# Kernel optimization log

Hardware: AMD Instinct MI355X
Metric: run time of the kernel (lower is better)

The kernel has to match this reference:

```python
import jax, jax.numpy as jnp
import numpy as np
from jax import lax

H = 2048          # hidden_size
T = 365           # history_length
F = 90            # future_u_length
TARGET_STEP = 30
RECOVER = 0.05
DEATH = 0.01


def setup_inputs() -> dict:
    key = jax.random.key(0)
    ks = jax.random.split(key, 14)
    s = 1.0 / np.sqrt(H)
    u = lambda k, shape: jax.random.uniform(k, shape, minval=-s, maxval=s, dtype=jnp.float32)
    return {
        "history_u": jax.random.uniform(ks[0], (1, 1, T), dtype=jnp.float32),
        "sird": jax.random.uniform(ks[1], (1, 1, 5), minval=0.5, maxval=1.5, dtype=jnp.float32),
        "target_step": TARGET_STEP,
        "Wb": u(ks[2], (H, 1)), "bb": u(ks[3], (H,)),
        "enc_Wih": u(ks[4], (3 * H, H)), "enc_Whh": u(ks[5], (3 * H, H)),
        "enc_bih": u(ks[6], (3 * H,)), "enc_bhh": u(ks[7], (3 * H,)),
        "dec_Wih": u(ks[8], (3 * H, H)), "dec_Whh": u(ks[9], (3 * H, H)),
        "dec_bih": u(ks[10], (3 * H,)), "dec_bhh": u(ks[11], (3 * H,)),
        "Wa": u(ks[12], (1, H)), "ba": u(ks[13], (1,)),
    }


def _gru_cell(x, h, Wih, Whh, bih, bhh):
    # PyTorch GRU cell math; x, h are [H] vectors.
    n = h.shape[0]
    gi = Wih @ x + bih            # [3H]
    gh = Whh @ h + bhh            # [3H]
    r = jax.nn.sigmoid(gi[:n] + gh[:n])
    z = jax.nn.sigmoid(gi[n:2 * n] + gh[n:2 * n])
    c = jnp.tanh(gi[2 * n:] + r * gh[2 * n:])
    return (1.0 - z) * c + z * h


def reference(history_u, sird, target_step, Wb, bb,
              enc_Wih, enc_Whh, enc_bih, enc_bhh,
              dec_Wih, dec_Whh, dec_bih, dec_bhh, Wa, ba):
    hsz = bb.shape[0]
    # Pre-projection of scalar inputs: [T, H]
    xs = history_u[0, 0][:, None] @ Wb.T + bb

    def enc_step(h, x):
        hp = _gru_cell(x, h, enc_Wih, enc_Whh, enc_bih, enc_bhh)
        # original applies sigmoid to hidden state between steps, keeps raw hp as y
        return jax.nn.sigmoid(hp), hp

    h_enc, ys = lax.scan(enc_step, jnp.zeros((hsz,), dtype=xs.dtype), xs)
    y = ys[-1]

    def dec_step(carry, _):
        y, h = carry
        hp = _gru_cell(y, h, dec_Wih, dec_Whh, dec_bih, dec_bhh)
        beta = jax.nn.sigmoid(hp @ Wa[0] + ba[0])   # scalar
        return (hp, hp), beta

    _, betas = lax.scan(dec_step, (y, h_enc), None, length=F)   # [F]

    def sird_update(x, beta):
        s, i, r, d, n = x[0], x[1], x[2], x[3], x[4]
        si = s * i * beta / n
        ir = i * RECOVER
        idd = i * DEATH
        return jnp.stack([s - si, i + si - ir - idd, r + ir, d + idd, n])

    x0 = sird[0, 0]
    xF = lax.scan(lambda x, b: (sird_update(x, b), None), x0, betas)[0]

    beta_last = betas[-1]

    def const_step(x, _):
        x2 = sird_update(x, beta_last)
        return x2, x2

    x_final, x_foo = lax.scan(const_step, xF, None, length=target_step - 1)
    return x_final.reshape(1, 1, 5), x_foo.reshape(-1, 1, 1, 5)
```

## Files before the change

kernel.cpp:

```cpp
#include <hip/hip_runtime.h>
#include <hip/hip_fp16.h>
#include <cstdint>
#include <cstddef>


#define HID   2048
#define T_ENC 365
#define F_DEC 90
#define NWG   256
#define NTH   512
#define SLOT  8192

#define WS_P    0
#define WS_Q    6144
#define WS_HBUF 12288
#define WS_DX0  45056
#define WS_HST  61440

typedef unsigned long long u64;

__device__ __forceinline__ float sigm(float x) {
    return 1.0f / (1.0f + __expf(-x));
}
__device__ __forceinline__ float tanh_f(float x) {
    return 1.0f - 2.0f / (1.0f + __expf(2.0f * x));
}
__device__ __forceinline__ unsigned bf16rne(float f) {
    unsigned x = __float_as_uint(f);
    return (x + 0x7fffu + ((x >> 16) & 1u)) >> 16;
}
__device__ __forceinline__ unsigned packbf(float lo, float hi) {
    return bf16rne(lo) | (bf16rne(hi) << 16);
}

__device__ __forceinline__ u64 tld(const u64* p) {
    return __hip_atomic_load((u64*)p, __ATOMIC_RELAXED, __HIP_MEMORY_SCOPE_AGENT);
}
__device__ __forceinline__ void tst(u64* p, u64 v) {
    __hip_atomic_store(p, v, __ATOMIC_RELAXED, __HIP_MEMORY_SCOPE_AGENT);
}
__device__ __forceinline__ u64 mk16(unsigned tag, float lo, float hi) {
    unsigned pk = (unsigned)__half_as_ushort(__float2half(lo)) |
                  ((unsigned)__half_as_ushort(__float2half(hi)) << 16);
    return ((u64)tag << 32) | (u64)pk;
}

__device__ __forceinline__ void poll_to_lds(const u64* __restrict__ rep,
                                            unsigned tag, int tid,
                                            float* __restrict__ lds) {
    const u64* p0 = rep + tid;
    const u64* p1 = rep + 512 + tid;
    u64 x0, x1;
    while (true) {
        x0 = tld(p0);
        x1 = tld(p1);
        bool ok = ((unsigned)(x0 >> 32) == tag) & ((unsigned)(x1 >> 32) == tag);
        if (__ballot(ok) == ~0ull) break;
    }
    unsigned lo0 = (unsigned)x0, lo1 = (unsigned)x1;
    float2 f0 = __half22float2(*(__half2*)&lo0);
    float2 f1 = __half22float2(*(__half2*)&lo1);
    *(float2*)(lds + 2 * tid) = f0;
    *(float2*)(lds + 1024 + 2 * tid) = f1;
}

__global__ void prep_pq(const float* __restrict__ Wih, const float* __restrict__ Wb,
                        const float* __restrict__ bb, const float* __restrict__ bih,
                        float* __restrict__ p, float* __restrict__ q) {
    int wave = threadIdx.x >> 6, lane = threadIdx.x & 63;
    int row = blockIdx.x * 4 + wave;
    const float* wr = Wih + (size_t)row * HID;
    float ap = 0.f, aq = 0.f;
    for (int k = lane; k < HID; k += 64) {
        float w = wr[k];
        ap += w * Wb[k];
        aq += w * bb[k];
    }
#pragma unroll
    for (int m = 1; m < 64; m <<= 1) {
        ap += __shfl_xor(ap, m);
        aq += __shfl_xor(aq, m);
    }
    if (lane == 0) {
        p[row] = ap;
        q[row] = aq + bih[row];
    }
}

__global__ __launch_bounds__(NTH, 1) void persist(
    const float* __restrict__ hu, const float* __restrict__ encWhh,
    const float* __restrict__ encBhh, const float* __restrict__ decWih,
    const float* __restrict__ decWhh, const float* __restrict__ decBih,
    const float* __restrict__ decBhh, const float* __restrict__ p,
    const float* __restrict__ q, u64* hbuf, u64* dx0, __half* hstore) {
    const int wg = blockIdx.x, tid = threadIdx.x;
    const int wave = tid >> 6, lane = tid & 63;
    const int j = wg * 8 + wave;
    const int myrep = wg & 7;

    __shared__ float h_lds[HID], x_lds[HID];
    __shared__ float hs_l[8], hy_l[8];
    __shared__ float p_l[24], q_l[24], ebhh[24], dbih[24], dbhh[24];
    __shared__ float u_l[T_ENC];

    for (int idx = tid; idx < T_ENC; idx += NTH) u_l[idx] = hu[idx];
    if (tid < 24) {
        int g = tid >> 3, jj = tid & 7;
        int r = g * HID + wg * 8 + jj;
        p_l[tid] = p[r];
        q_l[tid] = q[r];
        ebhh[tid] = encBhh[r];
        dbih[tid] = decBih[r];
        dbhh[tid] = decBhh[r];
    }

    float4 We[3][8];
#pragma unroll
    for (int g = 0; g < 3; g++) {
        const float* base = encWhh + (size_t)(g * HID + j) * HID;
#pragma unroll
        for (int i = 0; i < 8; i++)
            We[g][i] = *reinterpret_cast<const float4*>(base + 4 * lane + 256 * i);
    }

    for (int t = 0; t < T_ENC; t++) {
        if (t == 0) {
            for (int idx = tid; idx < HID; idx += NTH) h_lds[idx] = 0.f;
        } else {
            poll_to_lds(hbuf + (t & 1) * SLOT + myrep * 1024, (unsigned)t, tid,
                        h_lds);
        }
        __syncthreads();

        float4 hreg[8];
#pragma unroll
        for (int i = 0; i < 8; i++)
            hreg[i] = *reinterpret_cast<const float4*>(&h_lds[4 * lane + 256 * i]);

        float v0, v1, v2;
        {
            float a0 = 0.f, a1 = 0.f, a2 = 0.f, a3 = 0.f;
            float b0 = 0.f, b1 = 0.f, b2 = 0.f, b3 = 0.f;
            float c0 = 0.f, c1 = 0.f, c2 = 0.f, c3 = 0.f;
#pragma unroll
            for (int i = 0; i < 8; i++) {
                float4 h4 = hreg[i];
                float4 wr_ = We[0][i], wz_ = We[1][i], wc_ = We[2][i];
                a0 += wr_.x * h4.x; a1 += wr_.y * h4.y;
                a2 += wr_.z * h4.z; a3 += wr_.w * h4.w;
                b0 += wz_.x * h4.x; b1 += wz_.y * h4.y;
                b2 += wz_.z * h4.z; b3 += wz_.w * h4.w;
                c0 += wc_.x * h4.x; c1 += wc_.y * h4.y;
                c2 += wc_.z * h4.z; c3 += wc_.w * h4.w;
            }
            v0 = (a0 + a1) + (a2 + a3);
            v1 = (b0 + b1) + (b2 + b3);
            v2 = (c0 + c1) + (c2 + c3);
        }
#pragma unroll
        for (int m = 1; m < 64; m <<= 1) {
            v0 += __shfl_xor(v0, m);
            v1 += __shfl_xor(v1, m);
            v2 += __shfl_xor(v2, m);
        }

        if (lane == 0) {
            float u = u_l[t];
            float gir = u * p_l[wave] + q_l[wave];
            float giz = u * p_l[8 + wave] + q_l[8 + wave];
            float gic = u * p_l[16 + wave] + q_l[16 + wave];
            float r = sigm(gir + v0 + ebhh[wave]);
            float z = sigm(giz + v1 + ebhh[8 + wave]);
            float c = tanh_f(gic + r * (v2 + ebhh[16 + wave]));
            float hp = (1.f - z) * c + z * h_lds[j];
            hs_l[wave] = sigm(hp);
            hy_l[wave] = hp;
        }
        __syncthreads();
        if (wave == 0 && lane < 32) {
            int i = lane & 3, r = lane >> 2;
            u64 v = mk16((unsigned)(t + 1), hs_l[2 * i], hs_l[2 * i + 1]);
            tst(hbuf + ((t + 1) & 1) * SLOT + r * 1024 + wg * 4 + i, v);
            if (t == T_ENC - 1) {
                u64 y = mk16((unsigned)T_ENC, hy_l[2 * i], hy_l[2 * i + 1]);
                tst(dx0 + r * 1024 + wg * 4 + i, y);
            }
        }
    }

    unsigned Wd[6][8][2];
#pragma unroll
    for (int g = 0; g < 6; g++) {
        const float* src = (g < 3)
            ? decWih + (size_t)(g * HID + j) * HID
            : decWhh + (size_t)((g - 3) * HID + j) * HID;
#pragma unroll
        for (int i = 0; i < 8; i++) {
            float4 w = *reinterpret_cast<const float4*>(src + 4 * lane + 256 * i);
            Wd[g][i][0] = packbf(w.x, w.y);
            Wd[g][i][1] = packbf(w.z, w.w);
        }
    }

    for (int s = 0; s < F_DEC; s++) {
        unsigned rt = (unsigned)(T_ENC + s);
        poll_to_lds(hbuf + (rt & 1) * SLOT + myrep * 1024, rt, tid, h_lds);
        if (s == 0) poll_to_lds(dx0 + myrep * 1024, (unsigned)T_ENC, tid, x_lds);
        __syncthreads();

        const float* xs = (s == 0) ? x_lds : h_lds;
        float4 vx[8], vh[8];
#pragma unroll
        for (int i = 0; i < 8; i++) {
            vx[i] = *reinterpret_cast<const float4*>(&xs[4 * lane + 256 * i]);
            vh[i] = *reinterpret_cast<const float4*>(&h_lds[4 * lane + 256 * i]);
        }

        float d[6];
#pragma unroll
        for (int g = 0; g < 6; g++) {
            float a0 = 0.f, a1 = 0.f, a2 = 0.f, a3 = 0.f;
#pragma unroll
            for (int i = 0; i < 8; i++) {
                unsigned u0 = Wd[g][i][0], u1 = Wd[g][i][1];
                float4 v4 = (g < 3) ? vx[i] : vh[i];
                a0 += __uint_as_float(u0 << 16) * v4.x;
                a1 += __uint_as_float(u0 & 0xffff0000u) * v4.y;
                a2 += __uint_as_float(u1 << 16) * v4.z;
                a3 += __uint_as_float(u1 & 0xffff0000u) * v4.w;
            }
            d[g] = (a0 + a1) + (a2 + a3);
        }
#pragma unroll
        for (int m = 1; m < 64; m <<= 1) {
#pragma unroll
            for (int g = 0; g < 6; g++) d[g] += __shfl_xor(d[g], m);
        }

        if (lane == 0) {
            float r = sigm(d[0] + dbih[wave] + d[3] + dbhh[wave]);
            float z = sigm(d[1] + dbih[8 + wave] + d[4] + dbhh[8 + wave]);
            float c = tanh_f(d[2] + dbih[16 + wave] +
                             r * (d[5] + dbhh[16 + wave]));
            float hp = (1.f - z) * c + z * h_lds[j];
            hy_l[wave] = hp;
            hstore[s * HID + j] = __float2half(hp);
        }
        __syncthreads();
        if (wave == 0 && lane < 32) {
            int i = lane & 3, r = lane >> 2;
            u64 v = mk16(rt + 1, hy_l[2 * i], hy_l[2 * i + 1]);
            tst(hbuf + ((rt + 1) & 1) * SLOT + r * 1024 + wg * 4 + i, v);
        }
    }
}

__global__ void sird_k(const float* __restrict__ sird, const float* __restrict__ Wa,
                       const float* __restrict__ ba, const int* __restrict__ ts_p,
                       const __half* __restrict__ hstore, float* __restrict__ out) {
    __shared__ float bpre[96];
    int wave = threadIdx.x >> 6, lane = threadIdx.x & 63;
    const float4* wa4 = (const float4*)Wa;
    for (int s = wave; s < F_DEC; s += 8) {
        const uint4* hr = (const uint4*)(hstore + (size_t)s * HID);
        float acc = 0.f;
#pragma unroll
        for (int m = 0; m < 4; m++) {
            uint4 hh = hr[lane + 64 * m];
            float4 w0 = wa4[2 * (lane + 64 * m)];
            float4 w1 = wa4[2 * (lane + 64 * m) + 1];
            float2 f;
            f = __half22float2(*(__half2*)&hh.x);
            acc += w0.x * f.x + w0.y * f.y;
            f = __half22float2(*(__half2*)&hh.y);
            acc += w0.z * f.x + w0.w * f.y;
            f = __half22float2(*(__half2*)&hh.z);
            acc += w1.x * f.x + w1.y * f.y;
            f = __half22float2(*(__half2*)&hh.w);
            acc += w1.z * f.x + w1.w * f.y;
        }
#pragma unroll
        for (int m = 1; m < 64; m <<= 1) acc += __shfl_xor(acc, m);
        if (lane == 0) bpre[s] = acc;
    }
    __syncthreads();
    if (threadIdx.x == 0) {
        float s = sird[0], i = sird[1], r = sird[2], d = sird[3], n = sird[4];
        float bl = 0.f;
        for (int t = 0; t < F_DEC; t++) {
            float b = 1.f / (1.f + expf(-(bpre[t] + ba[0])));
            bl = b;
            float si = s * i * b / n, ir = i * 0.05f, id = i * 0.01f;
            s -= si;
            i += si - ir - id;
            r += ir;
            d += id;
        }
        int ts = ts_p[0];
        float* foo = out + 5;
        for (int t = 0; t < ts - 1; t++) {
            float si = s * i * bl / n, ir = i * 0.05f, id = i * 0.01f;
            s -= si;
            i += si - ir - id;
            r += ir;
            d += id;
            foo[t * 5 + 0] = s;
            foo[t * 5 + 1] = i;
            foo[t * 5 + 2] = r;
            foo[t * 5 + 3] = d;
            foo[t * 5 + 4] = n;
        }
        out[0] = s;
        out[1] = i;
        out[2] = r;
        out[3] = d;
        out[4] = n;
    }
}

extern "C" void kernel_launch(void* const* d_in, const int* in_sizes, int n_in,
                              void* d_out, int out_size, void* d_ws, size_t ws_size,
                              hipStream_t stream) {
    const float* hu = (const float*)d_in[0];
    const float* sird = (const float*)d_in[1];
    const int* ts = (const int*)d_in[2];
    const float* Wb = (const float*)d_in[3];
    const float* bb = (const float*)d_in[4];
    const float* eWih = (const float*)d_in[5];
    const float* eWhh = (const float*)d_in[6];
    const float* eBih = (const float*)d_in[7];
    const float* eBhh = (const float*)d_in[8];
    const float* dWih = (const float*)d_in[9];
    const float* dWhh = (const float*)d_in[10];
    const float* dBih = (const float*)d_in[11];
    const float* dBhh = (const float*)d_in[12];
    const float* Wa = (const float*)d_in[13];
    const float* ba = (const float*)d_in[14];

    float* wsf = (float*)d_ws;
    float* p = wsf + WS_P;
    float* q = wsf + WS_Q;
    u64* hbuf = (u64*)(wsf + WS_HBUF);
    u64* dx0 = (u64*)(wsf + WS_DX0);
    __half* hstore = (__half*)(wsf + WS_HST);

    hipLaunchKernelGGL(prep_pq, dim3(6144 / 4), dim3(256), 0, stream, eWih, Wb, bb,
                       eBih, p, q);
    hipLaunchKernelGGL(persist, dim3(NWG), dim3(NTH), 0, stream, hu, eWhh, eBhh,
                       dWih, dWhh, dBih, dBhh, p, q, hbuf, dx0, hstore);
    hipLaunchKernelGGL(sird_k, dim3(1), dim3(NTH), 0, stream, sird, Wa, ba, ts,
                       hstore, (float*)d_out);
}
```

Measured before the change: 1.796 ms.

## Use per-XCD leader workgroups to relay hidden state through local buffers

Each workgroup reads its XCD id from a hardware register and takes a slot from a per-XCD counter. The first workgroup on each XCD becomes a leader: it polls one global copy of the hidden state and re-publishes it into two XCD-local buffers with sc0 stores. The others poll those local copies with sc0 loads and fall back to the global buffer after a spin limit. Writers now publish a single copy instead of eight replicas. The aim is to cut cross-XCD coherence traffic during the per-step handoff, at the cost of an extra relay hop per step and a dependence on workgroups being spread evenly across XCDs.

```diff
diff --git a/kernel.cpp b/kernel.cpp
--- a/kernel.cpp
+++ b/kernel.cpp
@@ -9,13 +9,16 @@
 #define F_DEC 90
 #define NWG   256
 #define NTH   512
-#define SLOT  8192
+#define FB_SPIN 4096
 
 #define WS_P    0
 #define WS_Q    6144
-#define WS_HBUF 12288
-#define WS_DX0  45056
-#define WS_HST  61440
+#define WS_CTR  12288
+#define WS_GBUF 12296
+#define WS_GDX0 16392
+#define WS_LBUF 18440
+#define WS_LDX0 83976
+#define WS_HST  100360
 
 typedef unsigned long long u64;
 
@@ -39,17 +42,42 @@
 __device__ __forceinline__ void tst(u64* p, u64 v) {
     __hip_atomic_store(p, v, __ATOMIC_RELAXED, __HIP_MEMORY_SCOPE_AGENT);
 }
+__device__ __forceinline__ void ld2_sc0(const u64* p0, const u64* p1, u64& a,
+                                        u64& b) {
+    asm volatile(
+        "global_load_dwordx2 %0, %2, off sc0\n\t"
+        "global_load_dwordx2 %1, %3, off sc0\n\t"
+        "s_waitcnt vmcnt(0)"
+        : "=&v"(a), "=&v"(b)
+        : "v"(p0), "v"(p1)
+        : "memory");
+}
+__device__ __forceinline__ void st_sc0(u64* p, u64 v) {
+    asm volatile("global_store_dwordx2 %0, %1, off sc0" ::"v"(p), "v"(v)
+                 : "memory");
+}
+
 __device__ __forceinline__ u64 mk16(unsigned tag, float lo, float hi) {
     unsigned pk = (unsigned)__half_as_ushort(__float2half(lo)) |
                   ((unsigned)__half_as_ushort(__float2half(hi)) << 16);
     return ((u64)tag << 32) | (u64)pk;
 }
 
-__device__ __forceinline__ void poll_to_lds(const u64* __restrict__ rep,
-                                            unsigned tag, int tid,
-                                            float* __restrict__ lds) {
-    const u64* p0 = rep + tid;
-    const u64* p1 = rep + 512 + tid;
+__device__ __forceinline__ void unpack2(u64 x0, u64 x1, int tid,
+                                        float* __restrict__ lds) {
+    unsigned lo0 = (unsigned)x0, lo1 = (unsigned)x1;
+    float2 f0 = __half22float2(*(__half2*)&lo0);
+    float2 f1 = __half22float2(*(__half2*)&lo1);
+    *(float2*)(lds + 2 * tid) = f0;
+    *(float2*)(lds + 1024 + 2 * tid) = f1;
+}
+
+__device__ __forceinline__ void leader_step(const u64* __restrict__ g,
+                                            u64* __restrict__ l0,
+                                            u64* __restrict__ l1, unsigned tag,
+                                            int tid, float* __restrict__ lds) {
+    const u64* p0 = g + tid;
+    const u64* p1 = g + 512 + tid;
     u64 x0, x1;
     while (true) {
         x0 = tld(p0);
@@ -57,16 +85,53 @@
         bool ok = ((unsigned)(x0 >> 32) == tag) & ((unsigned)(x1 >> 32) == tag);
         if (__ballot(ok) == ~0ull) break;
     }
-    unsigned lo0 = (unsigned)x0, lo1 = (unsigned)x1;
-    float2 f0 = __half22float2(*(__half2*)&lo0);
-    float2 f1 = __half22float2(*(__half2*)&lo1);
-    *(float2*)(lds + 2 * tid) = f0;
-    *(float2*)(lds + 1024 + 2 * tid) = f1;
+    st_sc0(l0 + tid, x0);
+    st_sc0(l0 + 512 + tid, x1);
+    st_sc0(l1 + tid, x0);
+    st_sc0(l1 + 512 + tid, x1);
+    unpack2(x0, x1, tid, lds);
+}
+
+__device__ __forceinline__ void follower_step(const u64* __restrict__ l,
+                                              const u64* __restrict__ g,
+                                              unsigned tag, int tid,
+                                              float* __restrict__ lds,
+                                              bool& use_gb) {
+    u64 x0 = 0, x1 = 0;
+    if (!use_gb) {
+        const u64* p0 = l + tid;
+        const u64* p1 = l + 512 + tid;
+        int spins = 0;
+        while (true) {
+            ld2_sc0(p0, p1, x0, x1);
+            bool ok =
+                ((unsigned)(x0 >> 32) == tag) & ((unsigned)(x1 >> 32) == tag);
+            if (__ballot(ok) == ~0ull) break;
+            if (++spins > FB_SPIN) {
+                use_gb = true;
+                break;
+            }
+        }
+    }
+    if (use_gb) {
+        const u64* p0 = g + tid;
+        const u64* p1 = g + 512 + tid;
+        while (true) {
+            x0 = tld(p0);
+            x1 = tld(p1);
+            bool ok =
+                ((unsigned)(x0 >> 32) == tag) & ((unsigned)(x1 >> 32) == tag);
+            if (__ballot(ok) == ~0ull) break;
+        }
+    }
+    unpack2(x0, x1, tid, lds);
 }
 
 __global__ void prep_pq(const float* __restrict__ Wih, const float* __restrict__ Wb,
                         const float* __restrict__ bb, const float* __restrict__ bih,
-                        float* __restrict__ p, float* __restrict__ q) {
+                        float* __restrict__ p, float* __restrict__ q,
+                        int* __restrict__ ctr) {
+    if (blockIdx.x == 0 && threadIdx.x < 8) ctr[threadIdx.x] = 0;
     int wave = threadIdx.x >> 6, lane = threadIdx.x & 63;
     int row = blockIdx.x * 4 + wave;
     const float* wr = Wih + (size_t)row * HID;
@@ -92,16 +157,17 @@
     const float* __restrict__ encBhh, const float* __restrict__ decWih,
     const float* __restrict__ decWhh, const float* __restrict__ decBih,
     const float* __restrict__ decBhh, const float* __restrict__ p,
-    const float* __restrict__ q, u64* hbuf, u64* dx0, __half* hstore) {
+    const float* __restrict__ q, int* ctr, u64* gbuf, u64* gdx0, u64* lbuf,
+    u64* ldx0, __half* hstore) {
     const int wg = blockIdx.x, tid = threadIdx.x;
     const int wave = tid >> 6, lane = tid & 63;
     const int j = wg * 8 + wave;
-    const int myrep = wg & 7;
 
     __shared__ float h_lds[HID], x_lds[HID];
     __shared__ float hs_l[8], hy_l[8];
     __shared__ float p_l[24], q_l[24], ebhh[24], dbih[24], dbhh[24];
     __shared__ float u_l[T_ENC];
+    __shared__ int org_s[2];
 
     for (int idx = tid; idx < T_ENC; idx += NTH) u_l[idx] = hu[idx];
     if (tid < 24) {
@@ -113,6 +179,18 @@
         dbih[tid] = decBih[r];
         dbhh[tid] = decBhh[r];
     }
+    if (tid == 0) {
+        int xcd = (int)(__builtin_amdgcn_s_getreg((3 << 11) | 20)) & 7;
+        org_s[0] = xcd;
+        org_s[1] = atomicAdd(ctr + xcd, 1);
+    }
+    __syncthreads();
+    const int xcd = org_s[0];
+    const bool islead = (org_s[1] == 0);
+    const int myrep = org_s[1] & 1;
+    u64* lbx = lbuf + (size_t)xcd * 4096;
+    u64* lx0 = ldx0 + (size_t)xcd * 1024;
+    bool use_gb = false;
 
     float4 We[3][8];
 #pragma unroll
@@ -127,8 +205,14 @@
         if (t == 0) {
             for (int idx = tid; idx < HID; idx += NTH) h_lds[idx] = 0.f;
         } else {
-            poll_to_lds(hbuf + (t & 1) * SLOT + myrep * 1024, (unsigned)t, tid,
-                        h_lds);
+            const int slot = t & 1;
+            if (islead)
+                leader_step(gbuf + slot * 1024, lbx + slot * 2048,
+                            lbx + slot * 2048 + 1024, (unsigned)t, tid, h_lds);
+            else
+                follower_step(lbx + slot * 2048 + myrep * 1024,
+                              gbuf + slot * 1024, (unsigned)t, tid, h_lds,
+                              use_gb);
         }
         __syncthreads();
 
@@ -177,13 +261,12 @@
             hy_l[wave] = hp;
         }
         __syncthreads();
-        if (wave == 0 && lane < 32) {
-            int i = lane & 3, r = lane >> 2;
-            u64 v = mk16((unsigned)(t + 1), hs_l[2 * i], hs_l[2 * i + 1]);
-            tst(hbuf + ((t + 1) & 1) * SLOT + r * 1024 + wg * 4 + i, v);
+        if (wave == 0 && lane < 4) {
+            u64 v = mk16((unsigned)(t + 1), hs_l[2 * lane], hs_l[2 * lane + 1]);
+            tst(gbuf + ((t + 1) & 1) * 1024 + wg * 4 + lane, v);
             if (t == T_ENC - 1) {
-                u64 y = mk16((unsigned)T_ENC, hy_l[2 * i], hy_l[2 * i + 1]);
-                tst(dx0 + r * 1024 + wg * 4 + i, y);
+                u64 y = mk16((unsigned)T_ENC, hy_l[2 * lane], hy_l[2 * lane + 1]);
+                tst(gdx0 + wg * 4 + lane, y);
             }
         }
     }
@@ -204,8 +287,19 @@
 
     for (int s = 0; s < F_DEC; s++) {
         unsigned rt = (unsigned)(T_ENC + s);
-        poll_to_lds(hbuf + (rt & 1) * SLOT + myrep * 1024, rt, tid, h_lds);
-        if (s == 0) poll_to_lds(dx0 + myrep * 1024, (unsigned)T_ENC, tid, x_lds);
+        const int slot = rt & 1;
+        if (islead)
+            leader_step(gbuf + slot * 1024, lbx + slot * 2048,
+                        lbx + slot * 2048 + 1024, rt, tid, h_lds);
+        else
+            follower_step(lbx + slot * 2048 + myrep * 1024, gbuf + slot * 1024,
+                          rt, tid, h_lds, use_gb);
+        if (s == 0) {
+            if (islead)
+                leader_step(gdx0, lx0, lx0, (unsigned)T_ENC, tid, x_lds);
+            else
+                follower_step(lx0, gdx0, (unsigned)T_ENC, tid, x_lds, use_gb);
+        }
         __syncthreads();
 
         const float* xs = (s == 0) ? x_lds : h_lds;
@@ -247,10 +341,9 @@
             hstore[s * HID + j] = __float2half(hp);
         }
         __syncthreads();
-        if (wave == 0 && lane < 32) {
-            int i = lane & 3, r = lane >> 2;
-            u64 v = mk16(rt + 1, hy_l[2 * i], hy_l[2 * i + 1]);
-            tst(hbuf + ((rt + 1) & 1) * SLOT + r * 1024 + wg * 4 + i, v);
+        if (wave == 0 && lane < 4) {
+            u64 v = mk16(rt + 1, hy_l[2 * lane], hy_l[2 * lane + 1]);
+            tst(gbuf + ((rt + 1) & 1) * 1024 + wg * 4 + lane, v);
         }
     }
 }
@@ -340,14 +433,18 @@
     float* wsf = (float*)d_ws;
     float* p = wsf + WS_P;
     float* q = wsf + WS_Q;
-    u64* hbuf = (u64*)(wsf + WS_HBUF);
-    u64* dx0 = (u64*)(wsf + WS_DX0);
+    int* ctr = (int*)(wsf + WS_CTR);
+    u64* gbuf = (u64*)(wsf + WS_GBUF);
+    u64* gdx0 = (u64*)(wsf + WS_GDX0);
+    u64* lbuf = (u64*)(wsf + WS_LBUF);
+    u64* ldx0 = (u64*)(wsf + WS_LDX0);
     __half* hstore = (__half*)(wsf + WS_HST);
 
     hipLaunchKernelGGL(prep_pq, dim3(6144 / 4), dim3(256), 0, stream, eWih, Wb, bb,
-                       eBih, p, q);
+                       eBih, p, q, ctr);
     hipLaunchKernelGGL(persist, dim3(NWG), dim3(NTH), 0, stream, hu, eWhh, eBhh,
-                       dWih, dWhh, dBih, dBhh, p, q, hbuf, dx0, hstore);
+                       dWih, dWhh, dBih, dBhh, p, q, ctr, gbuf, gdx0, lbuf, ldx0,
+                       hstore);
     hipLaunchKernelGGL(sird_k, dim3(1), dim3(NTH), 0, stream, sird, Wa, ba, ts,
                        hstore, (float*)d_out);
 }
```

After: 2.778 ms. 1.55x slower.

## Publish hidden state per wave in fp32 and drop the second block barrier

Applied to the files above, without the earlier changes.

Each wave now computes the gate math on all lanes, keeps its own hidden element in a register, and writes tagged fp32 values straight to the replicated exchange buffer. This removes the per-step second __syncthreads and the LDS staging. Double-buffered LDS h arrays make the single remaining barrier safe. Polling now reads four u64 words per thread and re-polls only the lanes that are not ready. The trade-off is twice the exchange traffic and a larger replicated buffer, in exchange for fp32 precision instead of fp16.

```diff
diff --git a/kernel.cpp b/kernel.cpp
--- a/kernel.cpp
+++ b/kernel.cpp
@@ -9,13 +9,13 @@
 #define F_DEC 90
 #define NWG   256
 #define NTH   512
-#define SLOT  8192
+#define HBSZ  16384
 
 #define WS_P    0
 #define WS_Q    6144
 #define WS_HBUF 12288
-#define WS_DX0  45056
-#define WS_HST  61440
+#define WS_DX0  77824
+#define WS_HST  94208
 
 typedef unsigned long long u64;
 
@@ -39,10 +39,8 @@
 __device__ __forceinline__ void tst(u64* p, u64 v) {
     __hip_atomic_store(p, v, __ATOMIC_RELAXED, __HIP_MEMORY_SCOPE_AGENT);
 }
-__device__ __forceinline__ u64 mk16(unsigned tag, float lo, float hi) {
-    unsigned pk = (unsigned)__half_as_ushort(__float2half(lo)) |
-                  ((unsigned)__half_as_ushort(__float2half(hi)) << 16);
-    return ((u64)tag << 32) | (u64)pk;
+__device__ __forceinline__ u64 mkf(unsigned tag, float v) {
+    return ((u64)tag << 32) | (u64)__float_as_uint(v);
 }
 
 __device__ __forceinline__ void poll_to_lds(const u64* __restrict__ rep,
@@ -50,18 +48,23 @@
                                             float* __restrict__ lds) {
     const u64* p0 = rep + tid;
     const u64* p1 = rep + 512 + tid;
-    u64 x0, x1;
-    while (true) {
-        x0 = tld(p0);
-        x1 = tld(p1);
-        bool ok = ((unsigned)(x0 >> 32) == tag) & ((unsigned)(x1 >> 32) == tag);
-        if (__ballot(ok) == ~0ull) break;
-    }
-    unsigned lo0 = (unsigned)x0, lo1 = (unsigned)x1;
-    float2 f0 = __half22float2(*(__half2*)&lo0);
-    float2 f1 = __half22float2(*(__half2*)&lo1);
-    *(float2*)(lds + 2 * tid) = f0;
-    *(float2*)(lds + 1024 + 2 * tid) = f1;
+    const u64* p2 = rep + 1024 + tid;
+    const u64* p3 = rep + 1536 + tid;
+    u64 x0 = tld(p0), x1 = tld(p1), x2 = tld(p2), x3 = tld(p3);
+    bool k0 = ((unsigned)(x0 >> 32) == tag);
+    bool k1 = ((unsigned)(x1 >> 32) == tag);
+    bool k2 = ((unsigned)(x2 >> 32) == tag);
+    bool k3 = ((unsigned)(x3 >> 32) == tag);
+    while (__ballot(k0 & k1 & k2 & k3) != ~0ull) {
+        if (!k0) { x0 = tld(p0); k0 = ((unsigned)(x0 >> 32) == tag); }
+        if (!k1) { x1 = tld(p1); k1 = ((unsigned)(x1 >> 32) == tag); }
+        if (!k2) { x2 = tld(p2); k2 = ((unsigned)(x2 >> 32) == tag); }
+        if (!k3) { x3 = tld(p3); k3 = ((unsigned)(x3 >> 32) == tag); }
+    }
+    lds[tid] = __uint_as_float((unsigned)x0);
+    lds[512 + tid] = __uint_as_float((unsigned)x1);
+    lds[1024 + tid] = __uint_as_float((unsigned)x2);
+    lds[1536 + tid] = __uint_as_float((unsigned)x3);
 }
 
 __global__ void prep_pq(const float* __restrict__ Wih, const float* __restrict__ Wb,
@@ -98,8 +101,8 @@
     const int j = wg * 8 + wave;
     const int myrep = wg & 7;
 
-    __shared__ float h_lds[HID], x_lds[HID];
-    __shared__ float hs_l[8], hy_l[8];
+    __shared__ float h_l[2][HID];
+    __shared__ float x_lds[HID];
     __shared__ float p_l[24], q_l[24], ebhh[24], dbih[24], dbhh[24];
     __shared__ float u_l[T_ENC];
 
@@ -123,19 +126,22 @@
             We[g][i] = *reinterpret_cast<const float4*>(base + 4 * lane + 256 * i);
     }
 
+    float hcar = 0.f;
+
     for (int t = 0; t < T_ENC; t++) {
+        float* hb = h_l[t & 1];
         if (t == 0) {
-            for (int idx = tid; idx < HID; idx += NTH) h_lds[idx] = 0.f;
+            for (int idx = tid; idx < HID; idx += NTH) hb[idx] = 0.f;
         } else {
-            poll_to_lds(hbuf + (t & 1) * SLOT + myrep * 1024, (unsigned)t, tid,
-                        h_lds);
+            poll_to_lds(hbuf + (t & 1) * HBSZ + myrep * 2048, (unsigned)t, tid,
+                        hb);
         }
         __syncthreads();
 
         float4 hreg[8];
 #pragma unroll
         for (int i = 0; i < 8; i++)
-            hreg[i] = *reinterpret_cast<const float4*>(&h_lds[4 * lane + 256 * i]);
+            hreg[i] = *reinterpret_cast<const float4*>(&hb[4 * lane + 256 * i]);
 
         float v0, v1, v2;
         {
@@ -164,27 +170,21 @@
             v2 += __shfl_xor(v2, m);
         }
 
-        if (lane == 0) {
-            float u = u_l[t];
-            float gir = u * p_l[wave] + q_l[wave];
-            float giz = u * p_l[8 + wave] + q_l[8 + wave];
-            float gic = u * p_l[16 + wave] + q_l[16 + wave];
-            float r = sigm(gir + v0 + ebhh[wave]);
-            float z = sigm(giz + v1 + ebhh[8 + wave]);
-            float c = tanh_f(gic + r * (v2 + ebhh[16 + wave]));
-            float hp = (1.f - z) * c + z * h_lds[j];
-            hs_l[wave] = sigm(hp);
-            hy_l[wave] = hp;
-        }
-        __syncthreads();
-        if (wave == 0 && lane < 32) {
-            int i = lane & 3, r = lane >> 2;
-            u64 v = mk16((unsigned)(t + 1), hs_l[2 * i], hs_l[2 * i + 1]);
-            tst(hbuf + ((t + 1) & 1) * SLOT + r * 1024 + wg * 4 + i, v);
-            if (t == T_ENC - 1) {
-                u64 y = mk16((unsigned)T_ENC, hy_l[2 * i], hy_l[2 * i + 1]);
-                tst(dx0 + r * 1024 + wg * 4 + i, y);
-            }
+        float u = u_l[t];
+        float gir = u * p_l[wave] + q_l[wave];
+        float giz = u * p_l[8 + wave] + q_l[8 + wave];
+        float gic = u * p_l[16 + wave] + q_l[16 + wave];
+        float r = sigm(gir + v0 + ebhh[wave]);
+        float z = sigm(giz + v1 + ebhh[8 + wave]);
+        float c = tanh_f(gic + r * (v2 + ebhh[16 + wave]));
+        float hp = (1.f - z) * c + z * hcar;
+        float hs = sigm(hp);
+        hcar = hs;
+        if (lane < 8) {
+            tst(hbuf + ((t + 1) & 1) * HBSZ + lane * 2048 + j,
+                mkf((unsigned)(t + 1), hs));
+        } else if (t == T_ENC - 1 && lane < 12) {
+            tst(dx0 + (lane - 8) * 2048 + j, mkf((unsigned)T_ENC, hp));
         }
     }
 
@@ -204,16 +204,24 @@
 
     for (int s = 0; s < F_DEC; s++) {
         unsigned rt = (unsigned)(T_ENC + s);
-        poll_to_lds(hbuf + (rt & 1) * SLOT + myrep * 1024, rt, tid, h_lds);
-        if (s == 0) poll_to_lds(dx0 + myrep * 1024, (unsigned)T_ENC, tid, x_lds);
+        float* hb = h_l[rt & 1];
+        poll_to_lds(hbuf + (rt & 1) * HBSZ + myrep * 2048, rt, tid, hb);
+        if (s == 0)
+            poll_to_lds(dx0 + (wg & 3) * 2048, (unsigned)T_ENC, tid, x_lds);
         __syncthreads();
 
-        const float* xs = (s == 0) ? x_lds : h_lds;
         float4 vx[8], vh[8];
 #pragma unroll
-        for (int i = 0; i < 8; i++) {
-            vx[i] = *reinterpret_cast<const float4*>(&xs[4 * lane + 256 * i]);
-            vh[i] = *reinterpret_cast<const float4*>(&h_lds[4 * lane + 256 * i]);
+        for (int i = 0; i < 8; i++)
+            vh[i] = *reinterpret_cast<const float4*>(&hb[4 * lane + 256 * i]);
+        if (s == 0) {
+#pragma unroll
+            for (int i = 0; i < 8; i++)
+                vx[i] =
+                    *reinterpret_cast<const float4*>(&x_lds[4 * lane + 256 * i]);
+        } else {
+#pragma unroll
+            for (int i = 0; i < 8; i++) vx[i] = vh[i];
         }
 
         float d[6];
@@ -237,21 +245,15 @@
             for (int g = 0; g < 6; g++) d[g] += __shfl_xor(d[g], m);
         }
 
-        if (lane == 0) {
-            float r = sigm(d[0] + dbih[wave] + d[3] + dbhh[wave]);
-            float z = sigm(d[1] + dbih[8 + wave] + d[4] + dbhh[8 + wave]);
-            float c = tanh_f(d[2] + dbih[16 + wave] +
-                             r * (d[5] + dbhh[16 + wave]));
-            float hp = (1.f - z) * c + z * h_lds[j];
-            hy_l[wave] = hp;
-            hstore[s * HID + j] = __float2half(hp);
-        }
-        __syncthreads();
-        if (wave == 0 && lane < 32) {
-            int i = lane & 3, r = lane >> 2;
-            u64 v = mk16(rt + 1, hy_l[2 * i], hy_l[2 * i + 1]);
-            tst(hbuf + ((rt + 1) & 1) * SLOT + r * 1024 + wg * 4 + i, v);
-        }
+        float r = sigm(d[0] + dbih[wave] + d[3] + dbhh[wave]);
+        float z = sigm(d[1] + dbih[8 + wave] + d[4] + dbhh[8 + wave]);
+        float c = tanh_f(d[2] + dbih[16 + wave] + r * (d[5] + dbhh[16 + wave]));
+        float hp = (1.f - z) * c + z * hcar;
+        hcar = hp;
+        if (lane < 8) {
+            tst(hbuf + ((rt + 1) & 1) * HBSZ + lane * 2048 + j, mkf(rt + 1, hp));
+        }
+        if (lane == 0) hstore[s * HID + j] = __float2half(hp);
     }
 }
 
```

Measured after the change: 2.870 ms. 1.6x slower.

## Fuse input projection and SIRD tail into the persistent GRU kernel

Applied to the files above, without the earlier changes.

Folds the Wih·Wb / Wih·bb prologue into the persistent kernel, so each workgroup computes its own 24 rows before loading weights. It also computes each decoder beta dot product in workgroup 0 from the broadcast hidden state, and runs the SIRD recurrence at the end of the same kernel. This removes two extra kernel launches and the fp16 hidden-state store/reload. The costs are an extra serial prologue per workgroup reading the encoder Wih rows, and a small amount of extra work on the critical path of workgroup 0.

```diff
diff --git a/kernel.cpp b/kernel.cpp
--- a/kernel.cpp
+++ b/kernel.cpp
@@ -11,11 +11,8 @@
 #define NTH   512
 #define SLOT  8192
 
-#define WS_P    0
-#define WS_Q    6144
 #define WS_HBUF 12288
 #define WS_DX0  45056
-#define WS_HST  61440
 
 typedef unsigned long long u64;
 
@@ -64,35 +61,16 @@
     *(float2*)(lds + 1024 + 2 * tid) = f1;
 }
 
-__global__ void prep_pq(const float* __restrict__ Wih, const float* __restrict__ Wb,
-                        const float* __restrict__ bb, const float* __restrict__ bih,
-                        float* __restrict__ p, float* __restrict__ q) {
-    int wave = threadIdx.x >> 6, lane = threadIdx.x & 63;
-    int row = blockIdx.x * 4 + wave;
-    const float* wr = Wih + (size_t)row * HID;
-    float ap = 0.f, aq = 0.f;
-    for (int k = lane; k < HID; k += 64) {
-        float w = wr[k];
-        ap += w * Wb[k];
-        aq += w * bb[k];
-    }
-#pragma unroll
-    for (int m = 1; m < 64; m <<= 1) {
-        ap += __shfl_xor(ap, m);
-        aq += __shfl_xor(aq, m);
-    }
-    if (lane == 0) {
-        p[row] = ap;
-        q[row] = aq + bih[row];
-    }
-}
-
 __global__ __launch_bounds__(NTH, 1) void persist(
-    const float* __restrict__ hu, const float* __restrict__ encWhh,
+    const float* __restrict__ hu, const float* __restrict__ sird,
+    const int* __restrict__ ts_p, const float* __restrict__ Wb,
+    const float* __restrict__ bb, const float* __restrict__ encWih,
+    const float* __restrict__ encWhh, const float* __restrict__ encBih,
     const float* __restrict__ encBhh, const float* __restrict__ decWih,
     const float* __restrict__ decWhh, const float* __restrict__ decBih,
-    const float* __restrict__ decBhh, const float* __restrict__ p,
-    const float* __restrict__ q, u64* hbuf, u64* dx0, __half* hstore) {
+    const float* __restrict__ decBhh, const float* __restrict__ Wa,
+    const float* __restrict__ ba, u64* hbuf, u64* dx0,
+    float* __restrict__ out) {
     const int wg = blockIdx.x, tid = threadIdx.x;
     const int wave = tid >> 6, lane = tid & 63;
     const int j = wg * 8 + wave;
@@ -102,16 +80,46 @@
     __shared__ float hs_l[8], hy_l[8];
     __shared__ float p_l[24], q_l[24], ebhh[24], dbih[24], dbhh[24];
     __shared__ float u_l[T_ENC];
+    __shared__ float bpre_l[F_DEC];
 
     for (int idx = tid; idx < T_ENC; idx += NTH) u_l[idx] = hu[idx];
     if (tid < 24) {
         int g = tid >> 3, jj = tid & 7;
         int r = g * HID + wg * 8 + jj;
-        p_l[tid] = p[r];
-        q_l[tid] = q[r];
         ebhh[tid] = encBhh[r];
         dbih[tid] = decBih[r];
         dbhh[tid] = decBhh[r];
+    }
+
+    {
+        float ap[3], aq[3];
+#pragma unroll
+        for (int g = 0; g < 3; g++) {
+            const float* wr = encWih + (size_t)(g * HID + j) * HID;
+            float a = 0.f, b = 0.f;
+            for (int k = lane; k < HID; k += 64) {
+                float w = wr[k];
+                a += w * Wb[k];
+                b += w * bb[k];
+            }
+            ap[g] = a;
+            aq[g] = b;
+        }
+#pragma unroll
+        for (int m = 1; m < 64; m <<= 1) {
+#pragma unroll
+            for (int g = 0; g < 3; g++) {
+                ap[g] += __shfl_xor(ap[g], m);
+                aq[g] += __shfl_xor(aq[g], m);
+            }
+        }
+        if (lane == 0) {
+#pragma unroll
+            for (int g = 0; g < 3; g++) {
+                p_l[g * 8 + wave] = ap[g];
+                q_l[g * 8 + wave] = aq[g] + encBih[g * HID + j];
+            }
+        }
     }
 
     float4 We[3][8];
@@ -202,6 +210,13 @@
         }
     }
 
+    float4 waR[8];
+    if (wg == 0 && wave == 0) {
+#pragma unroll
+        for (int i = 0; i < 8; i++)
+            waR[i] = *reinterpret_cast<const float4*>(Wa + 4 * lane + 256 * i);
+    }
+
     for (int s = 0; s < F_DEC; s++) {
         unsigned rt = (unsigned)(T_ENC + s);
         poll_to_lds(hbuf + (rt & 1) * SLOT + myrep * 1024, rt, tid, h_lds);
@@ -214,6 +229,18 @@
         for (int i = 0; i < 8; i++) {
             vx[i] = *reinterpret_cast<const float4*>(&xs[4 * lane + 256 * i]);
             vh[i] = *reinterpret_cast<const float4*>(&h_lds[4 * lane + 256 * i]);
+        }
+
+        if (wg == 0 && wave == 0 && s > 0) {
+            float acc = 0.f;
+#pragma unroll
+            for (int i = 0; i < 8; i++) {
+                float4 w4 = waR[i], h4 = vh[i];
+                acc += w4.x * h4.x + w4.y * h4.y + w4.z * h4.z + w4.w * h4.w;
+            }
+#pragma unroll
+            for (int m = 1; m < 64; m <<= 1) acc += __shfl_xor(acc, m);
+            if (lane == 0) bpre_l[s - 1] = acc;
         }
 
         float d[6];
@@ -244,7 +271,6 @@
                              r * (d[5] + dbhh[16 + wave]));
             float hp = (1.f - z) * c + z * h_lds[j];
             hy_l[wave] = hp;
-            hstore[s * HID + j] = __float2half(hp);
         }
         __syncthreads();
         if (wave == 0 && lane < 32) {
@@ -253,68 +279,59 @@
             tst(hbuf + ((rt + 1) & 1) * SLOT + r * 1024 + wg * 4 + i, v);
         }
     }
-}
-
-__global__ void sird_k(const float* __restrict__ sird, const float* __restrict__ Wa,
-                       const float* __restrict__ ba, const int* __restrict__ ts_p,
-                       const __half* __restrict__ hstore, float* __restrict__ out) {
-    __shared__ float bpre[96];
-    int wave = threadIdx.x >> 6, lane = threadIdx.x & 63;
-    const float4* wa4 = (const float4*)Wa;
-    for (int s = wave; s < F_DEC; s += 8) {
-        const uint4* hr = (const uint4*)(hstore + (size_t)s * HID);
-        float acc = 0.f;
-#pragma unroll
-        for (int m = 0; m < 4; m++) {
-            uint4 hh = hr[lane + 64 * m];
-            float4 w0 = wa4[2 * (lane + 64 * m)];
-            float4 w1 = wa4[2 * (lane + 64 * m) + 1];
-            float2 f;
-            f = __half22float2(*(__half2*)&hh.x);
-            acc += w0.x * f.x + w0.y * f.y;
-            f = __half22float2(*(__half2*)&hh.y);
-            acc += w0.z * f.x + w0.w * f.y;
-            f = __half22float2(*(__half2*)&hh.z);
-            acc += w1.x * f.x + w1.y * f.y;
-            f = __half22float2(*(__half2*)&hh.w);
-            acc += w1.z * f.x + w1.w * f.y;
-        }
-#pragma unroll
-        for (int m = 1; m < 64; m <<= 1) acc += __shfl_xor(acc, m);
-        if (lane == 0) bpre[s] = acc;
-    }
-    __syncthreads();
-    if (threadIdx.x == 0) {
-        float s = sird[0], i = sird[1], r = sird[2], d = sird[3], n = sird[4];
-        float bl = 0.f;
-        for (int t = 0; t < F_DEC; t++) {
-            float b = 1.f / (1.f + expf(-(bpre[t] + ba[0])));
-            bl = b;
-            float si = s * i * b / n, ir = i * 0.05f, id = i * 0.01f;
-            s -= si;
-            i += si - ir - id;
-            r += ir;
-            d += id;
-        }
-        int ts = ts_p[0];
-        float* foo = out + 5;
-        for (int t = 0; t < ts - 1; t++) {
-            float si = s * i * bl / n, ir = i * 0.05f, id = i * 0.01f;
-            s -= si;
-            i += si - ir - id;
-            r += ir;
-            d += id;
-            foo[t * 5 + 0] = s;
-            foo[t * 5 + 1] = i;
-            foo[t * 5 + 2] = r;
-            foo[t * 5 + 3] = d;
-            foo[t * 5 + 4] = n;
-        }
-        out[0] = s;
-        out[1] = i;
-        out[2] = r;
-        out[3] = d;
-        out[4] = n;
+
+    if (wg == 0) {
+        poll_to_lds(hbuf + ((T_ENC + F_DEC) & 1) * SLOT + myrep * 1024,
+                    (unsigned)(T_ENC + F_DEC), tid, h_lds);
+        __syncthreads();
+        if (wave == 0) {
+            float acc = 0.f;
+#pragma unroll
+            for (int i = 0; i < 8; i++) {
+                float4 h4 =
+                    *reinterpret_cast<const float4*>(&h_lds[4 * lane + 256 * i]);
+                float4 w4 = waR[i];
+                acc += w4.x * h4.x + w4.y * h4.y + w4.z * h4.z + w4.w * h4.w;
+            }
+#pragma unroll
+            for (int m = 1; m < 64; m <<= 1) acc += __shfl_xor(acc, m);
+            if (lane == 0) bpre_l[F_DEC - 1] = acc;
+        }
+        __syncthreads();
+        if (tid == 0) {
+            float s = sird[0], i = sird[1], r = sird[2], d = sird[3],
+                  n = sird[4];
+            float ba0 = ba[0];
+            float bl = 0.f;
+            for (int t = 0; t < F_DEC; t++) {
+                float b = 1.f / (1.f + expf(-(bpre_l[t] + ba0)));
+                bl = b;
+                float si = s * i * b / n, ir = i * 0.05f, id = i * 0.01f;
+                s -= si;
+                i += si - ir - id;
+                r += ir;
+                d += id;
+            }
+            int ts = ts_p[0];
+            float* foo = out + 5;
+            for (int t = 0; t < ts - 1; t++) {
+                float si = s * i * bl / n, ir = i * 0.05f, id = i * 0.01f;
+                s -= si;
+                i += si - ir - id;
+                r += ir;
+                d += id;
+                foo[t * 5 + 0] = s;
+                foo[t * 5 + 1] = i;
+                foo[t * 5 + 2] = r;
+                foo[t * 5 + 3] = d;
+                foo[t * 5 + 4] = n;
+            }
+            out[0] = s;
+            out[1] = i;
+            out[2] = r;
+            out[3] = d;
+            out[4] = n;
+        }
     }
 }
 
@@ -338,16 +355,10 @@
     const float* ba = (const float*)d_in[14];
 
     float* wsf = (float*)d_ws;
-    float* p = wsf + WS_P;
-    float* q = wsf + WS_Q;
     u64* hbuf = (u64*)(wsf + WS_HBUF);
     u64* dx0 = (u64*)(wsf + WS_DX0);
-    __half* hstore = (__half*)(wsf + WS_HST);
-
-    hipLaunchKernelGGL(prep_pq, dim3(6144 / 4), dim3(256), 0, stream, eWih, Wb, bb,
-                       eBih, p, q);
-    hipLaunchKernelGGL(persist, dim3(NWG), dim3(NTH), 0, stream, hu, eWhh, eBhh,
-                       dWih, dWhh, dBih, dBhh, p, q, hbuf, dx0, hstore);
-    hipLaunchKernelGGL(sird_k, dim3(1), dim3(NTH), 0, stream, sird, Wa, ba, ts,
-                       hstore, (float*)d_out);
-}
+
+    hipLaunchKernelGGL(persist, dim3(NWG), dim3(NTH), 0, stream, hu, sird, ts,
+                       Wb, bb, eWih, eWhh, eBih, eBhh, dWih, dWhh, dBih, dBhh,
+                       Wa, ba, hbuf, dx0, (float*)d_out);
+}
```

After: 2.634 ms. 1.47x slower.
